# Kernel optimization log

Hardware: AMD Instinct MI355X
Metric: run time of the kernel (lower is better)

Reference implementation:

```python
import jax, jax.numpy as jnp
import numpy as np

B, P, T = 16, 65536, 64
THRESHOLD = 0.5
VAR_XY, VAR_WH = 0.1, 0.2  # standard SSD encode variances used by match()


def _rand_boxes(key, shape_prefix):
    k1, k2 = jax.random.split(key)
    xy = jax.random.uniform(k1, shape_prefix + (2,), dtype=jnp.float32) * 0.8
    wh = jax.random.uniform(k2, shape_prefix + (2,), dtype=jnp.float32) * 0.18 + 0.02
    return jnp.concatenate([xy, xy + wh], axis=-1)  # valid corner-form boxes in [0,1]


def setup_inputs() -> dict:
    key = jax.random.key(0)
    k1, k2, k3, k4 = jax.random.split(key, 4)
    return {
        "loc_data": jax.random.normal(k1, (B, P, 4), dtype=jnp.float32),
        "conf_data": jax.random.normal(k2, (B, P, 2), dtype=jnp.float32),
        "anchors": _rand_boxes(k3, (B, P)),
        "targets": _rand_boxes(k4, (B, T)),
    }


def _match_one(truths, anchors):
    # truths: [T,4], anchors: [P,4], both corner form (x1,y1,x2,y2)
    area_t = (truths[:, 2] - truths[:, 0]) * (truths[:, 3] - truths[:, 1])  # [T]
    area_a = (anchors[:, 2] - anchors[:, 0]) * (anchors[:, 3] - anchors[:, 1])  # [P]
    lt = jnp.maximum(truths[:, None, :2], anchors[None, :, :2])
    rb = jnp.minimum(truths[:, None, 2:], anchors[None, :, 2:])
    wh = jnp.clip(rb - lt, 0.0)
    inter = wh[..., 0] * wh[..., 1]  # [T,P] -- dominant memory traffic
    iou = inter / (area_t[:, None] + area_a[None, :] - inter)

    best_prior_idx = jnp.argmax(iou, axis=1)  # [T] best anchor per truth
    best_truth_overlap = jnp.max(iou, axis=0)  # [P]
    best_truth_idx = jnp.argmax(iou, axis=0)  # [P]
    # force-match each truth's best anchor (SSD match())
    best_truth_overlap = best_truth_overlap.at[best_prior_idx].set(2.0)
    best_truth_idx = best_truth_idx.at[best_prior_idx].set(jnp.arange(truths.shape[0]))

    matches = truths[best_truth_idx]  # [P,4]
    conf = (best_truth_overlap >= THRESHOLD).astype(jnp.int32)  # binary labels

    # encode matched boxes w.r.t. anchors (center-size form)
    a_cxcy = (anchors[:, :2] + anchors[:, 2:]) * 0.5
    a_wh = anchors[:, 2:] - anchors[:, :2]
    m_cxcy = (matches[:, :2] + matches[:, 2:]) * 0.5
    m_wh = matches[:, 2:] - matches[:, :2]
    g_cxcy = (m_cxcy - a_cxcy) / (VAR_XY * a_wh)
    g_wh = jnp.log(m_wh / a_wh) / VAR_WH
    loc_t = jnp.concatenate([g_cxcy, g_wh], axis=-1)  # [P,4]
    return loc_t, conf


def reference(loc_data, conf_data, anchors, targets):
    # vectorized over images (the torch code loops over the batch index column)
    loc_t, conf_t = jax.vmap(_match_one)(targets, anchors)  # [B,P,4], [B,P]
    pos = conf_t > 0  # [B,P]

    # smooth-L1 (beta=1) summed over positive anchors
    diff = loc_data - loc_t
    ad = jnp.abs(diff)
    sl1 = jnp.where(ad < 1.0, 0.5 * ad * ad, ad - 0.5)
    loss_l = jnp.sum(sl1 * pos[..., None].astype(sl1.dtype))
    cnt_l = jnp.sum(pos).astype(sl1.dtype)

    # cross-entropy: per-image mean (torch default reduction), summed, then / total count
    logp = jax.nn.log_softmax(conf_data, axis=-1)  # [B,P,2]
    ce = -jnp.take_along_axis(logp, conf_t[..., None], axis=-1)[..., 0]  # [B,P]
    loss_c = jnp.sum(jnp.mean(ce, axis=1)) / (conf_data.shape[0] * conf_data.shape[1])

    return loss_l / cnt_l + loss_c
```

## Files before the change

### kernel.cpp

```cpp
#include <hip/hip_runtime.h>

#define B_ 16
#define P_ 65536
#define T_ 64
#define APT 4
#define BLK 256
#define APB (APT * BLK)
#define NBLK (P_ / APB)
#define NPART (B_ * NBLK)

__device__ __forceinline__ float rcpf(float x) { return __builtin_amdgcn_rcpf(x); }

template <int CTRL>
__device__ __forceinline__ unsigned dpp_mov(unsigned v) {
    return (unsigned)__builtin_amdgcn_update_dpp((int)v, (int)v, CTRL, 0xf, 0xf, false);
}
template <int CTRL>
__device__ __forceinline__ unsigned long long dpp_key(unsigned long long k) {
    unsigned lo = dpp_mov<CTRL>((unsigned)k);
    unsigned hi = dpp_mov<CTRL>((unsigned)(k >> 32));
    return ((unsigned long long)hi << 32) | lo;
}
__device__ __forceinline__ unsigned long long wave_max_key(unsigned long long k) {
    unsigned long long o;
    o = dpp_key<0x111>(k); k = (o > k) ? o : k;
    o = dpp_key<0x112>(k); k = (o > k) ? o : k;
    o = dpp_key<0x114>(k); k = (o > k) ? o : k;
    o = dpp_key<0x118>(k); k = (o > k) ? o : k;
    o = dpp_key<0x142>(k); k = (o > k) ? o : k;
    o = dpp_key<0x143>(k); k = (o > k) ? o : k;
    return k;
}

__device__ __forceinline__ void iou_iu(const float4& a, float aa, const float4& tb,
                                       float at, float& inter, float& u) {
    float lx = fmaxf(tb.x, a.x), ly = fmaxf(tb.y, a.y);
    float rx = fminf(tb.z, a.z), ry = fminf(tb.w, a.w);
    float w = fmaxf(__fsub_rn(rx, lx), 0.0f);
    float h = fmaxf(__fsub_rn(ry, ly), 0.0f);
    inter = __fmul_rn(w, h);
    u     = __fsub_rn(__fadd_rn(at, aa), inter);
}

__device__ __forceinline__ bool gt_iou(float i1, float u1, float i2, float u2) {
    return __fmul_rn(i1, u2) > __fmul_rn(i2, u1);
}

__device__ __forceinline__ float sl1(float d) {
    float ad = fabsf(d);
    return (ad < 1.0f) ? 0.5f * ad * ad : ad - 0.5f;
}

__device__ __forceinline__ float sl1_enc(const float4& l, const float4& a, const float4& m) {
    float aw = a.z - a.x, ah = a.w - a.y;
    float acx = (a.x + a.z) * 0.5f, acy = (a.y + a.w) * 0.5f;
    float mcx = (m.x + m.z) * 0.5f, mcy = (m.y + m.w) * 0.5f;
    float mw = m.z - m.x, mh = m.w - m.y;
    float g0 = (mcx - acx) / (0.1f * aw);
    float g1 = (mcy - acy) / (0.1f * ah);
    float g2 = __logf(mw / aw) * 5.0f;
    float g3 = __logf(mh / ah) * 5.0f;
    return sl1(l.x - g0) + sl1(l.y - g1) + sl1(l.z - g2) + sl1(l.w - g3);
}

__global__ __launch_bounds__(256) void k1(const float4* __restrict__ loc,
                                          const float2* __restrict__ conf,
                                          const float4* __restrict__ anchors,
                                          const float4* __restrict__ targets,
                                          unsigned long long* __restrict__ best_blk,
                                          float4* __restrict__ part) {
    const int b    = blockIdx.y;
    const int bx   = blockIdx.x;
    const int tid  = threadIdx.x;
    const int base = bx * APB;

    __shared__ float4 tt[T_];
    __shared__ float  ta[T_];
    __shared__ unsigned long long arr[4][T_];
    if (tid < T_) {
        float4 t = targets[b * T_ + tid];
        tt[tid] = t;
        ta[tid] = (t.z - t.x) * (t.w - t.y);
    }
    __syncthreads();

    float4 a[APT]; float aa[APT]; int p[APT];
#pragma unroll
    for (int i = 0; i < APT; ++i) {
        p[i]  = base + i * BLK + tid;
        a[i]  = anchors[(size_t)b * P_ + p[i]];
        aa[i] = (a[i].z - a[i].x) * (a[i].w - a[i].y);
    }

    float ib[APT], ub[APT]; int bt[APT];
#pragma unroll
    for (int i = 0; i < APT; ++i) { ib[i] = 0.0f; ub[i] = 1.0f; bt[i] = 0; }

    for (int t = 0; t < T_; ++t) {
        const float4 tb = tt[t];
        const float  at = ta[t];
        float li = 0.0f, lu = 1.0f; int lp = 0;
#pragma unroll
        for (int i = 0; i < APT; ++i) {
            float inter, u;
            iou_iu(a[i], aa[i], tb, at, inter, u);
            if (gt_iou(inter, u, ib[i], ub[i])) { ib[i] = inter; ub[i] = u; bt[i] = t; }
            if (gt_iou(inter, u, li, lu)) { li = inter; lu = u; lp = p[i]; }
        }
        float iou = __fmul_rn(li, rcpf(lu));
        unsigned long long key =
            ((unsigned long long)__float_as_uint(iou) << 32) |
            (unsigned long long)(0xFFFFFFFFu - (unsigned)lp);
        key = wave_max_key(key);
        if ((tid & 63) == 63) arr[tid >> 6][t] = key;
    }
    __syncthreads();

    if (tid < T_) {
        unsigned long long k = arr[0][tid];
        k = (arr[1][tid] > k) ? arr[1][tid] : k;
        k = (arr[2][tid] > k) ? arr[2][tid] : k;
        k = (arr[3][tid] > k) ? arr[3][tid] : k;
        best_blk[(size_t)(b * NBLK + bx) * T_ + tid] = k;
    }

    float ll = 0.0f, cn = 0.0f, ces = 0.0f;
#pragma unroll
    for (int i = 0; i < APT; ++i) {
        int lab = (__fmul_rn(2.0f, ib[i]) >= ub[i]);
        float2 c = conf[(size_t)b * P_ + p[i]];
        float mx  = fmaxf(c.x, c.y);
        float lse = mx + __logf(__expf(c.x - mx) + __expf(c.y - mx));
        ces += lse - (lab ? c.y : c.x);
        if (lab) {
            float4 l = loc[(size_t)b * P_ + p[i]];
            ll += sl1_enc(l, a[i], tt[bt[i]]);
            cn += 1.0f;
        }
    }
#pragma unroll
    for (int off = 32; off; off >>= 1) {
        ll  += __shfl_down(ll,  off, 64);
        cn  += __shfl_down(cn,  off, 64);
        ces += __shfl_down(ces, off, 64);
    }
    __shared__ float r[3][4];
    const int lane = tid & 63, w = tid >> 6;
    if (lane == 0) { r[0][w] = ll; r[1][w] = cn; r[2][w] = ces; }
    __syncthreads();
    if (tid == 0) {
        part[b * NBLK + bx] = make_float4(r[0][0] + r[0][1] + r[0][2] + r[0][3],
                                          r[1][0] + r[1][1] + r[1][2] + r[1][3],
                                          r[2][0] + r[2][1] + r[2][2] + r[2][3], 0.0f);
    }
}

__global__ __launch_bounds__(1024) void k2(const float4* __restrict__ loc,
                                           const float2* __restrict__ conf,
                                           const float4* __restrict__ anchors,
                                           const float4* __restrict__ targets,
                                           const unsigned long long* __restrict__ best_blk,
                                           const float4* __restrict__ part,
                                           float* __restrict__ out) {
    const int tid = threadIdx.x;
    const int b = tid >> 6, t = tid & 63;

    __shared__ float4   tt[B_][T_];
    __shared__ float    ta[B_][T_];
    __shared__ unsigned bp[B_][T_];
    __shared__ float    red[3][16];
    __shared__ float    dacc[3];
    if (tid < 3) dacc[tid] = 0.0f;

    float4 tb0 = targets[tid];
    tt[b][t] = tb0;
    ta[b][t] = (tb0.z - tb0.x) * (tb0.w - tb0.y);

    unsigned long long k = 0ull;
    for (int blk = 0; blk < NBLK; ++blk) {
        unsigned long long o = best_blk[(size_t)(b * NBLK + blk) * T_ + t];
        k = (o > k) ? o : k;
    }
    bp[b][t] = 0xFFFFFFFFu - (unsigned)(k & 0xFFFFFFFFull);

    float4 pr = part[tid];
    float ll = pr.x, cn = pr.y, ces = pr.z;
#pragma unroll
    for (int off = 32; off; off >>= 1) {
        ll  += __shfl_down(ll,  off, 64);
        cn  += __shfl_down(cn,  off, 64);
        ces += __shfl_down(ces, off, 64);
    }
    if ((tid & 63) == 0) { red[0][tid >> 6] = ll; red[1][tid >> 6] = cn; red[2][tid >> 6] = ces; }
    __syncthreads();

    float dll = 0.0f, dcn = 0.0f, dce = 0.0f;
    const unsigned mine = bp[b][t];
    bool dup = false;
    for (int t2 = t + 1; t2 < T_; ++t2) dup |= (bp[b][t2] == mine);
    if (!dup) {
        const int pidx = (int)mine;
        const float4 a  = anchors[(size_t)b * P_ + pidx];
        const float  aa = (a.z - a.x) * (a.w - a.y);
        float ibv = 0.0f, ubv = 1.0f; int btv = 0;
        for (int t2 = 0; t2 < T_; ++t2) {
            float inter, u;
            iou_iu(a, aa, tt[b][t2], ta[b][t2], inter, u);
            if (gt_iou(inter, u, ibv, ubv)) { ibv = inter; ubv = u; btv = t2; }
        }
        int lab_old = (__fmul_rn(2.0f, ibv) >= ubv);
        float2 c = conf[(size_t)b * P_ + pidx];
        dce = (lab_old ? c.y : c.x) - c.y;
        float4 l = loc[(size_t)b * P_ + pidx];
        dll = sl1_enc(l, a, tt[b][t]);
        if (lab_old) dll -= sl1_enc(l, a, tt[b][btv]);
        dcn = lab_old ? 0.0f : 1.0f;
    }
#pragma unroll
    for (int off = 32; off; off >>= 1) {
        dll += __shfl_down(dll, off, 64);
        dcn += __shfl_down(dcn, off, 64);
        dce += __shfl_down(dce, off, 64);
    }
    if ((tid & 63) == 0) {
        atomicAdd(&dacc[0], dll);
        atomicAdd(&dacc[1], dcn);
        atomicAdd(&dacc[2], dce);
    }
    __syncthreads();

    if (tid == 0) {
        double L = 0.0, C = 0.0, E = 0.0;
        for (int w = 0; w < 16; ++w) { L += red[0][w]; C += red[1][w]; E += red[2][w]; }
        L += dacc[0]; C += dacc[1]; E += dacc[2];
        out[0] = (float)(L / C + E / ((double)P_ * (double)(B_ * P_)));
    }
}

extern "C" void kernel_launch(void* const* d_in, const int* in_sizes, int n_in,
                              void* d_out, int out_size, void* d_ws, size_t ws_size,
                              hipStream_t stream) {
    const float4* loc     = (const float4*)d_in[0];
    const float2* conf    = (const float2*)d_in[1];
    const float4* anchors = (const float4*)d_in[2];
    const float4* targets = (const float4*)d_in[3];

    unsigned long long* best_blk = (unsigned long long*)d_ws;
    float4* part = (float4*)((char*)d_ws + (size_t)B_ * NBLK * T_ * sizeof(unsigned long long));

    dim3 g1(NBLK, B_);
    k1<<<g1, dim3(BLK), 0, stream>>>(loc, conf, anchors, targets, best_blk, part);

    k2<<<dim3(1), dim3(1024), 0, stream>>>(loc, conf, anchors, targets, best_blk, part,
                                           (float*)d_out);
}
```

Measured before the change: 164.5 us.

## Double anchors per thread and replace 64-bit wave argmax with 32-bit max plus ballot

```diff
diff --git a/kernel.cpp b/kernel.cpp
--- a/kernel.cpp
+++ b/kernel.cpp
@@ -3,7 +3,7 @@
 #define B_ 16
 #define P_ 65536
 #define T_ 64
-#define APT 4
+#define APT 8
 #define BLK 256
 #define APB (APT * BLK)
 #define NBLK (P_ / APB)
@@ -15,21 +15,25 @@
 __device__ __forceinline__ unsigned dpp_mov(unsigned v) {
     return (unsigned)__builtin_amdgcn_update_dpp((int)v, (int)v, CTRL, 0xf, 0xf, false);
 }
-template <int CTRL>
-__device__ __forceinline__ unsigned long long dpp_key(unsigned long long k) {
-    unsigned lo = dpp_mov<CTRL>((unsigned)k);
-    unsigned hi = dpp_mov<CTRL>((unsigned)(k >> 32));
-    return ((unsigned long long)hi << 32) | lo;
-}
-__device__ __forceinline__ unsigned long long wave_max_key(unsigned long long k) {
-    unsigned long long o;
-    o = dpp_key<0x111>(k); k = (o > k) ? o : k;
-    o = dpp_key<0x112>(k); k = (o > k) ? o : k;
-    o = dpp_key<0x114>(k); k = (o > k) ? o : k;
-    o = dpp_key<0x118>(k); k = (o > k) ? o : k;
-    o = dpp_key<0x142>(k); k = (o > k) ? o : k;
-    o = dpp_key<0x143>(k); k = (o > k) ? o : k;
-    return k;
+__device__ __forceinline__ unsigned wave_max_u32(unsigned v) {
+    unsigned o;
+    o = dpp_mov<0x111>(v); v = (o > v) ? o : v;
+    o = dpp_mov<0x112>(v); v = (o > v) ? o : v;
+    o = dpp_mov<0x114>(v); v = (o > v) ? o : v;
+    o = dpp_mov<0x118>(v); v = (o > v) ? o : v;
+    o = dpp_mov<0x142>(v); v = (o > v) ? o : v;
+    o = dpp_mov<0x143>(v); v = (o > v) ? o : v;
+    return v;
+}
+__device__ __forceinline__ unsigned wave_min_u32(unsigned v) {
+    unsigned o;
+    o = dpp_mov<0x111>(v); v = (o < v) ? o : v;
+    o = dpp_mov<0x112>(v); v = (o < v) ? o : v;
+    o = dpp_mov<0x114>(v); v = (o < v) ? o : v;
+    o = dpp_mov<0x118>(v); v = (o < v) ? o : v;
+    o = dpp_mov<0x142>(v); v = (o < v) ? o : v;
+    o = dpp_mov<0x143>(v); v = (o < v) ? o : v;
+    return v;
 }
 
 __device__ __forceinline__ void iou_iu(const float4& a, float aa, const float4& tb,
@@ -84,11 +88,10 @@
     }
     __syncthreads();
 
-    float4 a[APT]; float aa[APT]; int p[APT];
+    float4 a[APT]; float aa[APT];
 #pragma unroll
     for (int i = 0; i < APT; ++i) {
-        p[i]  = base + i * BLK + tid;
-        a[i]  = anchors[(size_t)b * P_ + p[i]];
+        a[i]  = anchors[(size_t)b * P_ + (base + i * BLK + tid)];
         aa[i] = (a[i].z - a[i].x) * (a[i].w - a[i].y);
     }
 
@@ -96,23 +99,34 @@
 #pragma unroll
     for (int i = 0; i < APT; ++i) { ib[i] = 0.0f; ub[i] = 1.0f; bt[i] = 0; }
 
+#pragma unroll 2
     for (int t = 0; t < T_; ++t) {
         const float4 tb = tt[t];
         const float  at = ta[t];
-        float li = 0.0f, lu = 1.0f; int lp = 0;
+        float li = 0.0f, lu = 1.0f; unsigned lp = 0u;
 #pragma unroll
         for (int i = 0; i < APT; ++i) {
             float inter, u;
             iou_iu(a[i], aa[i], tb, at, inter, u);
             if (gt_iou(inter, u, ib[i], ub[i])) { ib[i] = inter; ub[i] = u; bt[i] = t; }
-            if (gt_iou(inter, u, li, lu)) { li = inter; lu = u; lp = p[i]; }
-        }
-        float iou = __fmul_rn(li, rcpf(lu));
-        unsigned long long key =
-            ((unsigned long long)__float_as_uint(iou) << 32) |
-            (unsigned long long)(0xFFFFFFFFu - (unsigned)lp);
-        key = wave_max_key(key);
-        if ((tid & 63) == 63) arr[tid >> 6][t] = key;
+            if (gt_iou(inter, u, li, lu)) { li = inter; lu = u; lp = (unsigned)(base + i * BLK + tid); }
+        }
+        unsigned bits = __float_as_uint(__fmul_rn(li, rcpf(lu)));
+        unsigned m    = wave_max_u32(bits);
+        unsigned smax = (unsigned)__builtin_amdgcn_readlane((int)m, 63);
+        unsigned long long mask = __ballot(bits == smax);
+        unsigned lpw;
+        if (__popcll(mask) == 1) {
+            int winner = __ffsll((long long)mask) - 1;
+            lpw = (unsigned)__builtin_amdgcn_readlane((int)lp, winner);
+        } else {
+            unsigned cand = (bits == smax) ? lp : 0xFFFFFFFFu;
+            unsigned mn = wave_min_u32(cand);
+            lpw = (unsigned)__builtin_amdgcn_readlane((int)mn, 63);
+        }
+        if ((tid & 63) == 0)
+            arr[tid >> 6][t] = ((unsigned long long)smax << 32) |
+                               (unsigned long long)(0xFFFFFFFFu - lpw);
     }
     __syncthreads();
 
@@ -128,12 +142,12 @@
 #pragma unroll
     for (int i = 0; i < APT; ++i) {
         int lab = (__fmul_rn(2.0f, ib[i]) >= ub[i]);
-        float2 c = conf[(size_t)b * P_ + p[i]];
+        float2 c = conf[(size_t)b * P_ + (base + i * BLK + tid)];
         float mx  = fmaxf(c.x, c.y);
         float lse = mx + __logf(__expf(c.x - mx) + __expf(c.y - mx));
         ces += lse - (lab ? c.y : c.x);
         if (lab) {
-            float4 l = loc[(size_t)b * P_ + p[i]];
+            float4 l = loc[(size_t)b * P_ + (base + i * BLK + tid)];
             ll += sl1_enc(l, a[i], tt[bt[i]]);
             cn += 1.0f;
         }
@@ -183,8 +197,11 @@
     }
     bp[b][t] = 0xFFFFFFFFu - (unsigned)(k & 0xFFFFFFFFull);
 
-    float4 pr = part[tid];
-    float ll = pr.x, cn = pr.y, ces = pr.z;
+    float ll = 0.0f, cn = 0.0f, ces = 0.0f;
+    if (tid < NPART) {
+        float4 pr = part[tid];
+        ll = pr.x; cn = pr.y; ces = pr.z;
+    }
 #pragma unroll
     for (int off = 32; off; off >>= 1) {
         ll  += __shfl_down(ll,  off, 64);
```

Measured after the change: 159.2 us. 1.03x faster.

## Compute per-truth best anchor via lane-per-truth scan over LDS anchors

Applied to the files above, without the earlier changes.

```diff
diff --git a/kernel.cpp b/kernel.cpp
--- a/kernel.cpp
+++ b/kernel.cpp
@@ -8,29 +8,9 @@
 #define APB (APT * BLK)
 #define NBLK (P_ / APB)
 #define NPART (B_ * NBLK)
+#define WCH (APB / 4)
 
 __device__ __forceinline__ float rcpf(float x) { return __builtin_amdgcn_rcpf(x); }
-
-template <int CTRL>
-__device__ __forceinline__ unsigned dpp_mov(unsigned v) {
-    return (unsigned)__builtin_amdgcn_update_dpp((int)v, (int)v, CTRL, 0xf, 0xf, false);
-}
-template <int CTRL>
-__device__ __forceinline__ unsigned long long dpp_key(unsigned long long k) {
-    unsigned lo = dpp_mov<CTRL>((unsigned)k);
-    unsigned hi = dpp_mov<CTRL>((unsigned)(k >> 32));
-    return ((unsigned long long)hi << 32) | lo;
-}
-__device__ __forceinline__ unsigned long long wave_max_key(unsigned long long k) {
-    unsigned long long o;
-    o = dpp_key<0x111>(k); k = (o > k) ? o : k;
-    o = dpp_key<0x112>(k); k = (o > k) ? o : k;
-    o = dpp_key<0x114>(k); k = (o > k) ? o : k;
-    o = dpp_key<0x118>(k); k = (o > k) ? o : k;
-    o = dpp_key<0x142>(k); k = (o > k) ? o : k;
-    o = dpp_key<0x143>(k); k = (o > k) ? o : k;
-    return k;
-}
 
 __device__ __forceinline__ void iou_iu(const float4& a, float aa, const float4& tb,
                                        float at, float& inter, float& u) {
@@ -74,23 +54,27 @@
     const int tid  = threadIdx.x;
     const int base = bx * APB;
 
+    __shared__ float4 sa[APB];
+    __shared__ float  saa[APB];
     __shared__ float4 tt[T_];
     __shared__ float  ta[T_];
     __shared__ unsigned long long arr[4][T_];
+
     if (tid < T_) {
         float4 t = targets[b * T_ + tid];
         tt[tid] = t;
         ta[tid] = (t.z - t.x) * (t.w - t.y);
     }
-    __syncthreads();
-
-    float4 a[APT]; float aa[APT]; int p[APT];
+
+    float4 a[APT]; float aa[APT];
 #pragma unroll
     for (int i = 0; i < APT; ++i) {
-        p[i]  = base + i * BLK + tid;
-        a[i]  = anchors[(size_t)b * P_ + p[i]];
+        a[i]  = anchors[(size_t)b * P_ + (base + i * BLK + tid)];
         aa[i] = (a[i].z - a[i].x) * (a[i].w - a[i].y);
-    }
+        sa[i * BLK + tid]  = a[i];
+        saa[i * BLK + tid] = aa[i];
+    }
+    __syncthreads();
 
     float ib[APT], ub[APT]; int bt[APT];
 #pragma unroll
@@ -99,20 +83,31 @@
     for (int t = 0; t < T_; ++t) {
         const float4 tb = tt[t];
         const float  at = ta[t];
-        float li = 0.0f, lu = 1.0f; int lp = 0;
 #pragma unroll
         for (int i = 0; i < APT; ++i) {
             float inter, u;
             iou_iu(a[i], aa[i], tb, at, inter, u);
             if (gt_iou(inter, u, ib[i], ub[i])) { ib[i] = inter; ub[i] = u; bt[i] = t; }
-            if (gt_iou(inter, u, li, lu)) { li = inter; lu = u; lp = p[i]; }
+        }
+    }
+
+    {
+        const int w    = tid >> 6;
+        const int lane = tid & 63;
+        const float4 mytb = tt[lane];
+        const float  myat = ta[lane];
+        float li = 0.0f, lu = 1.0f; unsigned lp = 0u;
+#pragma unroll 4
+        for (int j = w * WCH; j < w * WCH + WCH; ++j) {
+            float4 aj = sa[j];
+            float aaj = saa[j];
+            float inter, u;
+            iou_iu(aj, aaj, mytb, myat, inter, u);
+            if (gt_iou(inter, u, li, lu)) { li = inter; lu = u; lp = (unsigned)(base + j); }
         }
         float iou = __fmul_rn(li, rcpf(lu));
-        unsigned long long key =
-            ((unsigned long long)__float_as_uint(iou) << 32) |
-            (unsigned long long)(0xFFFFFFFFu - (unsigned)lp);
-        key = wave_max_key(key);
-        if ((tid & 63) == 63) arr[tid >> 6][t] = key;
+        arr[w][lane] = ((unsigned long long)__float_as_uint(iou) << 32) |
+                       (unsigned long long)(0xFFFFFFFFu - lp);
     }
     __syncthreads();
 
@@ -128,12 +123,12 @@
 #pragma unroll
     for (int i = 0; i < APT; ++i) {
         int lab = (__fmul_rn(2.0f, ib[i]) >= ub[i]);
-        float2 c = conf[(size_t)b * P_ + p[i]];
+        float2 c = conf[(size_t)b * P_ + (base + i * BLK + tid)];
         float mx  = fmaxf(c.x, c.y);
         float lse = mx + __logf(__expf(c.x - mx) + __expf(c.y - mx));
         ces += lse - (lab ? c.y : c.x);
         if (lab) {
-            float4 l = loc[(size_t)b * P_ + p[i]];
+            float4 l = loc[(size_t)b * P_ + (base + i * BLK + tid)];
             ll += sl1_enc(l, a[i], tt[bt[i]]);
             cn += 1.0f;
         }
```

Result: slower. 167.8 us (+2.0%).
